# Kernel optimization log

Measured on AMD Instinct MI355X. Metric: run time of the kernel, lower is better.

The kernel has to match this reference:

```python
import jax, jax.numpy as jnp
import numpy as np

N_NODES = 100000
N_EDGES = 1600000
N_GRAPHS = 512
F_IN = 20
HID = 128
OUT = HID // 2


def _glorot(key, shape):
    fan_in, fan_out = shape[0], shape[1]
    lim = float(np.sqrt(6.0 / (fan_in + fan_out)))
    return jax.random.uniform(key, shape, jnp.float32, -lim, lim)


def setup_inputs() -> dict:
    key = jax.random.key(0)
    ks = jax.random.split(key, 12)
    x = jax.random.normal(ks[0], (N_NODES, F_IN), jnp.float32)
    edge_index = jax.random.randint(ks[1], (2, N_EDGES), 0, N_NODES, dtype=jnp.int64)
    batch = jnp.sort(jax.random.randint(ks[2], (N_NODES,), 0, N_GRAPHS, dtype=jnp.int64))
    return {
        "x": x,
        "edge_index": edge_index,
        "batch": batch,
        "W1": _glorot(ks[3], (F_IN, HID)), "b1": jnp.zeros((HID,), jnp.float32),
        "W2": _glorot(ks[4], (HID, HID)), "b2": jnp.zeros((HID,), jnp.float32),
        "W3": _glorot(ks[5], (HID, HID)), "b3": jnp.zeros((HID,), jnp.float32),
        "Wout": _glorot(ks[6], (HID, OUT)), "bout": jnp.zeros((OUT,), jnp.float32),
    }


def _gcn_conv(x, W, b, src, dst, num_nodes):
    # PyG GCNConv: x' = D^{-1/2} (A + I) D^{-1/2} X W + b (self-loops already in src/dst)
    xw = x @ W                                                  # [N, H]
    ones = jnp.ones(src.shape[0], dtype=xw.dtype)
    deg = jax.ops.segment_sum(ones, dst, num_segments=num_nodes)
    dinv = jnp.where(deg > 0, jax.lax.rsqrt(deg), 0.0)          # [N]
    norm = dinv[src] * dinv[dst]                                # [E+N]
    msg = xw[src] * norm[:, None]                               # gather + scale
    return jax.ops.segment_sum(msg, dst, num_segments=num_nodes) + b


def reference(x, edge_index, batch, W1, b1, W2, b2, W3, b3, Wout, bout):
    num_nodes = x.shape[0]
    loops = jnp.arange(num_nodes, dtype=edge_index.dtype)
    src = jnp.concatenate([edge_index[0], loops])
    dst = jnp.concatenate([edge_index[1], loops])

    h = jax.nn.relu(_gcn_conv(x, W1, b1, src, dst, num_nodes))
    h = jax.nn.relu(_gcn_conv(h, W2, b2, src, dst, num_nodes))
    h = jax.nn.relu(_gcn_conv(h, W3, b3, src, dst, num_nodes))

    # global_mean_pool over graph ids
    sums = jax.ops.segment_sum(h, batch, num_segments=N_GRAPHS)
    counts = jax.ops.segment_sum(jnp.ones(num_nodes, h.dtype), batch, num_segments=N_GRAPHS)
    pooled = sums / jnp.maximum(counts, 1.0)[:, None]           # [G, H]
    return pooled @ Wout + bout                                 # [G, H//2]
```

## Files before the change

kernel.cpp:

```cpp
#include <hip/hip_runtime.h>
#include <hip/hip_fp16.h>

#define N_NODES 100000
#define N_EDGES 1600000
#define N_GRAPHS 512
#define F_IN 20
#define HID 128
#define OUT_F 64

#define BUCKETS 256
#define SPAN 391
#define BCAP 7000
#define EPB 4096

typedef _Float16 half8_t __attribute__((ext_vector_type(8)));
typedef float f32x4_t __attribute__((ext_vector_type(4)));

__device__ inline float4 h4_to_f4(uint2 u) {
    __half2 h0 = *(__half2*)&u.x;
    __half2 h1 = *(__half2*)&u.y;
    float2 f0 = __half22float2(h0);
    float2 f1 = __half22float2(h1);
    return make_float4(f0.x, f0.y, f1.x, f1.y);
}

__global__ __launch_bounds__(512) void partition(const int* __restrict__ src,
                                                 const int* __restrict__ dst,
                                                 int* __restrict__ bpairs,
                                                 int* cur256) {
    __shared__ int lcnt[8][BUCKETS];
    __shared__ int woff[8][BUCKETS];
    int t = threadIdx.x;
    int wv = t >> 6;
    for (int i = t; i < 8 * BUCKETS; i += 512) ((int*)lcnt)[i] = 0;
    __syncthreads();
    int base = blockIdx.x * EPB;
    int myb[8], myp[8], myr[8];
#pragma unroll
    for (int i = 0; i < 8; ++i) {
        int e = base + i * 512 + t;
        int b = -1, p = 0, rk = 0;
        if (e < N_EDGES) {
            int s = src[e], d = dst[e];
            b = d / SPAN;
            p = (s << 9) | (d - b * SPAN);
            rk = atomicAdd(&lcnt[wv][b], 1);
        }
        myb[i] = b; myp[i] = p; myr[i] = rk;
    }
    __syncthreads();
    if (t < BUCKETS) {
        int c[8], tot = 0;
#pragma unroll
        for (int w = 0; w < 8; ++w) { c[w] = lcnt[w][t]; tot += c[w]; }
        int gb = atomicAdd(&cur256[t], tot);
#pragma unroll
        for (int w = 0; w < 8; ++w) { woff[w][t] = gb; gb += c[w]; }
    }
    __syncthreads();
#pragma unroll
    for (int i = 0; i < 8; ++i) {
        int b = myb[i];
        if (b >= 0) {
            int p = woff[wv][b] + myr[i];
            if (p < BCAP) bpairs[(size_t)b * BCAP + p] = myp[i];
        }
    }
}

__global__ __launch_bounds__(512) void csr_build(const int* __restrict__ bpairs,
                                                 const int* __restrict__ cur256,
                                                 int* __restrict__ row_st,
                                                 int* __restrict__ csr,
                                                 const float* __restrict__ x,
                                                 __half* __restrict__ Xs) {
    __shared__ int ocnt[SPAN];
    __shared__ int sc[512];
    __shared__ int cur[SPAN];
    __shared__ int sbase;
    int b = blockIdx.x, t = threadIdx.x;

    int myc = (t < BUCKETS) ? cur256[t] : 0;
    sc[t] = myc;
    __syncthreads();
    for (int o = 1; o < BUCKETS; o <<= 1) {
        int v = (t >= o) ? sc[t - o] : 0;
        __syncthreads();
        sc[t] += v;
        __syncthreads();
    }
    if (t == b) sbase = sc[t] - myc;
    if (b == BUCKETS - 1 && t == 0) row_st[N_NODES] = N_EDGES;

    int n0 = b * SPAN;
    int span = N_NODES - n0; if (span > SPAN) span = SPAN;
    if (t < SPAN) ocnt[t] = 0;
    __syncthreads();

    int n = cur256[b];
    const int* p = bpairs + (size_t)b * BCAP;
    for (int i = t; i < n; i += 512) atomicAdd(&ocnt[p[i] & 511], 1);
    __syncthreads();
    sc[t] = (t < span) ? ocnt[t] : 0;
    __syncthreads();
    for (int o = 1; o < 512; o <<= 1) {
        int v = (t >= o) ? sc[t - o] : 0;
        __syncthreads();
        sc[t] += v;
        __syncthreads();
    }
    int base = sbase;
    if (t < span) {
        int start = sc[t] - ocnt[t];
        row_st[n0 + t] = base + start;
        cur[t] = start;
    }
    __syncthreads();
    for (int i = t; i < n; i += 512) {
        int e = p[i];
        int lp = atomicAdd(&cur[e & 511], 1);
        csr[base + lp] = e >> 9;
    }
    for (int i = t; i < span * 32; i += 512) {
        int nl = i >> 5, f = i & 31;
        float v = (f < F_IN) ? x[(size_t)(n0 + nl) * F_IN + f] : 0.f;
        float di = rsqrtf((float)(ocnt[nl] + 1));
        Xs[(size_t)(n0 + nl) * 32 + f] = __float2half(di * v);
    }
}

__global__ __launch_bounds__(256) void layer1(const __half* __restrict__ Xs,
                                              const int* __restrict__ row_st,
                                              const int* __restrict__ csr,
                                              const float* __restrict__ W,
                                              const float* __restrict__ bias,
                                              __half* __restrict__ H) {
    __shared__ float Wlds[F_IN * HID];
    __shared__ float Alds[16 * F_IN];
    const int t = threadIdx.x;
    const int node0 = blockIdx.x * 16;

    for (int i = t; i < F_IN * HID; i += 256) Wlds[i] = W[i];

    const int h16 = t >> 4;
    const int l16 = t & 15;
    const __half2* X2 = (const __half2*)Xs;
    {
        int nn = node0 + h16;
        int r0 = row_st[nn], r1 = row_st[nn + 1];
        float2 f = __half22float2(X2[(size_t)nn * 16 + l16]);
        float2 acc = f;
        int r = r0;
        for (; r + 1 < r1; r += 2) {
            float2 f0 = __half22float2(X2[(size_t)csr[r] * 16 + l16]);
            float2 f1 = __half22float2(X2[(size_t)csr[r + 1] * 16 + l16]);
            acc.x += f0.x + f1.x;
            acc.y += f0.y + f1.y;
        }
        if (r < r1) {
            float2 f2 = __half22float2(X2[(size_t)csr[r] * 16 + l16]);
            acc.x += f2.x; acc.y += f2.y;
        }
        if (l16 < 10) {
            float di = rsqrtf((float)(r1 - r0 + 1));
            Alds[h16 * F_IN + l16 * 2]     = di * acc.x;
            Alds[h16 * F_IN + l16 * 2 + 1] = di * acc.y;
        }
    }
    __syncthreads();

    const int g  = t >> 5;
    const int h4 = (t & 31) * 4;
    float4 b4 = *(const float4*)&bias[h4];
    float4 acc0 = b4;
    float4 acc1 = b4;
#pragma unroll
    for (int kk = 0; kk < F_IN; ++kk) {
        float a0 = Alds[(g * 2) * F_IN + kk];
        float a1 = Alds[(g * 2 + 1) * F_IN + kk];
        float4 w = *(const float4*)&Wlds[kk * HID + h4];
        acc0.x = fmaf(a0, w.x, acc0.x);
        acc0.y = fmaf(a0, w.y, acc0.y);
        acc0.z = fmaf(a0, w.z, acc0.z);
        acc0.w = fmaf(a0, w.w, acc0.w);
        acc1.x = fmaf(a1, w.x, acc1.x);
        acc1.y = fmaf(a1, w.y, acc1.y);
        acc1.z = fmaf(a1, w.z, acc1.z);
        acc1.w = fmaf(a1, w.w, acc1.w);
    }
    {
        __half2 h0 = __floats2half2_rn(acc0.x, acc0.y);
        __half2 h1 = __floats2half2_rn(acc0.z, acc0.w);
        uint2 u; u.x = *(unsigned*)&h0; u.y = *(unsigned*)&h1;
        ((uint2*)H)[(node0 + g * 2) * 32 + (h4 >> 2)] = u;
    }
    {
        __half2 h0 = __floats2half2_rn(acc1.x, acc1.y);
        __half2 h1 = __floats2half2_rn(acc1.z, acc1.w);
        uint2 u; u.x = *(unsigned*)&h0; u.y = *(unsigned*)&h1;
        ((uint2*)H)[(node0 + g * 2 + 1) * 32 + (h4 >> 2)] = u;
    }
}

__global__ __launch_bounds__(256) void gemm_mfma(const __half* __restrict__ H,
                                                 const float* __restrict__ W,
                                                 const int* __restrict__ row_st,
                                                 __half* __restrict__ T) {
    __shared__ _Float16 Whi[64 * 128];
    __shared__ _Float16 Wlo[64 * 128];
    const int t = threadIdx.x;
    const int c0 = (blockIdx.x & 1) * 64;

    for (int i = t; i < 128 * 64; i += 256) {
        int k = i >> 6, c = i & 63;
        float w = W[k * HID + c0 + c];
        _Float16 hi = (_Float16)w;
        _Float16 lo = (_Float16)((w - (float)hi) * 2048.0f);
        int addr = c * 128 + (((k >> 3) ^ (c & 15)) << 3) + (k & 7);
        Whi[addr] = hi;
        Wlo[addr] = lo;
    }
    __syncthreads();

    const int wv = t >> 6;
    const int l  = t & 63;
    const int lr = l & 15;
    const int lq = l >> 4;

    for (int rep = 0; rep < 4; ++rep) {
        int strip = ((blockIdx.x >> 1) * 4 + wv) * 4 + rep;
        if (strip >= N_NODES / 16) continue;
        int n0 = strip * 16;

        f32x4_t acc[4], acl[4];
#pragma unroll
        for (int ct = 0; ct < 4; ++ct) { acc[ct] = (f32x4_t){0,0,0,0}; acl[ct] = (f32x4_t){0,0,0,0}; }

#pragma unroll
        for (int kc = 0; kc < 4; ++kc) {
            half8_t a = *(const half8_t*)(H + (size_t)(n0 + lr) * 128 + kc * 32 + lq * 8);
#pragma unroll
            for (int j = 0; j < 8; ++j) a[j] = a[j] > (_Float16)0 ? a[j] : (_Float16)0;
            int g = kc * 4 + lq;
#pragma unroll
            for (int ct = 0; ct < 4; ++ct) {
                int c = ct * 16 + lr;
                int addr = c * 128 + ((g ^ lr) << 3);
                half8_t bh = *(const half8_t*)&Whi[addr];
                half8_t bl = *(const half8_t*)&Wlo[addr];
                acc[ct] = __builtin_amdgcn_mfma_f32_16x16x32_f16(a, bh, acc[ct], 0, 0, 0);
                acl[ct] = __builtin_amdgcn_mfma_f32_16x16x32_f16(a, bl, acl[ct], 0, 0, 0);
            }
        }

        int r0 = n0 + lq * 4;
#pragma unroll
        for (int r = 0; r < 4; ++r) {
            int row = r0 + r;
            float d = rsqrtf((float)(row_st[row + 1] - row_st[row] + 1));
#pragma unroll
            for (int ct = 0; ct < 4; ++ct) {
                float v = (acc[ct][r] + acl[ct][r] * 4.8828125e-4f) * d;
                T[(size_t)row * 128 + c0 + ct * 16 + lr] = __float2half(v);
            }
        }
    }
}

__global__ __launch_bounds__(256) void gather_range(const __half* __restrict__ A,
                                                    const int* __restrict__ row_st,
                                                    const int* __restrict__ csr,
                                                    const float* __restrict__ bias,
                                                    __half* __restrict__ B) {
    int t = threadIdx.x;
    int n = blockIdx.x * 8 + (t >> 5);
    int l = t & 31;
    int r0 = row_st[n], r1 = row_st[n + 1];
    float di = rsqrtf((float)(r1 - r0 + 1));
    const uint2* Af = (const uint2*)A;
    float4 acc = h4_to_f4(Af[n * 32 + l]);
    int r = r0;
    for (; r + 7 < r1; r += 8) {
        int s0 = csr[r],     s1 = csr[r + 1], s2 = csr[r + 2], s3 = csr[r + 3];
        int s4 = csr[r + 4], s5 = csr[r + 5], s6 = csr[r + 6], s7 = csr[r + 7];
        float4 v0 = h4_to_f4(Af[s0 * 32 + l]);
        float4 v1 = h4_to_f4(Af[s1 * 32 + l]);
        float4 v2 = h4_to_f4(Af[s2 * 32 + l]);
        float4 v3 = h4_to_f4(Af[s3 * 32 + l]);
        float4 v4 = h4_to_f4(Af[s4 * 32 + l]);
        float4 v5 = h4_to_f4(Af[s5 * 32 + l]);
        float4 v6 = h4_to_f4(Af[s6 * 32 + l]);
        float4 v7 = h4_to_f4(Af[s7 * 32 + l]);
        acc.x += ((v0.x + v1.x) + (v2.x + v3.x)) + ((v4.x + v5.x) + (v6.x + v7.x));
        acc.y += ((v0.y + v1.y) + (v2.y + v3.y)) + ((v4.y + v5.y) + (v6.y + v7.y));
        acc.z += ((v0.z + v1.z) + (v2.z + v3.z)) + ((v4.z + v5.z) + (v6.z + v7.z));
        acc.w += ((v0.w + v1.w) + (v2.w + v3.w)) + ((v4.w + v5.w) + (v6.w + v7.w));
    }
    for (; r + 3 < r1; r += 4) {
        int s0 = csr[r], s1 = csr[r + 1], s2 = csr[r + 2], s3 = csr[r + 3];
        float4 v0 = h4_to_f4(Af[s0 * 32 + l]);
        float4 v1 = h4_to_f4(Af[s1 * 32 + l]);
        float4 v2 = h4_to_f4(Af[s2 * 32 + l]);
        float4 v3 = h4_to_f4(Af[s3 * 32 + l]);
        acc.x += (v0.x + v1.x) + (v2.x + v3.x);
        acc.y += (v0.y + v1.y) + (v2.y + v3.y);
        acc.z += (v0.z + v1.z) + (v2.z + v3.z);
        acc.w += (v0.w + v1.w) + (v2.w + v3.w);
    }
    for (; r < r1; ++r) {
        float4 v = h4_to_f4(Af[csr[r] * 32 + l]);
        acc.x += v.x; acc.y += v.y; acc.z += v.z; acc.w += v.w;
    }
    float4 b4 = ((const float4*)bias)[l];
    __half2 h0 = __floats2half2_rn(fmaf(di, acc.x, b4.x), fmaf(di, acc.y, b4.y));
    __half2 h1 = __floats2half2_rn(fmaf(di, acc.z, b4.z), fmaf(di, acc.w, b4.w));
    uint2 u; u.x = *(unsigned*)&h0; u.y = *(unsigned*)&h1;
    ((uint2*)B)[n * 32 + l] = u;
}

__global__ __launch_bounds__(256) void gather_pool(const __half* __restrict__ A,
                                                   const int* __restrict__ row_st,
                                                   const int* __restrict__ csr,
                                                   const float* __restrict__ bias,
                                                   const int* __restrict__ batch,
                                                   float* sums, float* counts) {
    int t = threadIdx.x;
    int l = t & 31;
    int n0 = (blockIdx.x * 8 + (t >> 5)) * 8;
    if (n0 >= N_NODES) return;
    const uint2* Af = (const uint2*)A;
    float4 b4 = ((const float4*)bias)[l];
    int cur = batch[n0];
    int runlen = 0;
    float4 pacc = make_float4(0.f, 0.f, 0.f, 0.f);
    for (int k = 0; k < 8; ++k) {
        int n = n0 + k;
        if (n >= N_NODES) break;
        int g = batch[n];
        if (g != cur) {
            float* sp = &sums[cur * HID + l * 4];
            atomicAdd(sp + 0, pacc.x); atomicAdd(sp + 1, pacc.y);
            atomicAdd(sp + 2, pacc.z); atomicAdd(sp + 3, pacc.w);
            if (l == 0) atomicAdd(&counts[cur], (float)runlen);
            pacc = make_float4(0.f, 0.f, 0.f, 0.f);
            runlen = 0;
            cur = g;
        }
        int r0 = row_st[n], r1 = row_st[n + 1];
        float4 acc = h4_to_f4(Af[n * 32 + l]);
        int r = r0;
        for (; r + 7 < r1; r += 8) {
            int s0 = csr[r],     s1 = csr[r + 1], s2 = csr[r + 2], s3 = csr[r + 3];
            int s4 = csr[r + 4], s5 = csr[r + 5], s6 = csr[r + 6], s7 = csr[r + 7];
            float4 v0 = h4_to_f4(Af[s0 * 32 + l]);
            float4 v1 = h4_to_f4(Af[s1 * 32 + l]);
            float4 v2 = h4_to_f4(Af[s2 * 32 + l]);
            float4 v3 = h4_to_f4(Af[s3 * 32 + l]);
            float4 v4 = h4_to_f4(Af[s4 * 32 + l]);
            float4 v5 = h4_to_f4(Af[s5 * 32 + l]);
            float4 v6 = h4_to_f4(Af[s6 * 32 + l]);
            float4 v7 = h4_to_f4(Af[s7 * 32 + l]);
            acc.x += ((v0.x + v1.x) + (v2.x + v3.x)) + ((v4.x + v5.x) + (v6.x + v7.x));
            acc.y += ((v0.y + v1.y) + (v2.y + v3.y)) + ((v4.y + v5.y) + (v6.y + v7.y));
            acc.z += ((v0.z + v1.z) + (v2.z + v3.z)) + ((v4.z + v5.z) + (v6.z + v7.z));
            acc.w += ((v0.w + v1.w) + (v2.w + v3.w)) + ((v4.w + v5.w) + (v6.w + v7.w));
        }
        for (; r + 3 < r1; r += 4) {
            int s0 = csr[r], s1 = csr[r + 1], s2 = csr[r + 2], s3 = csr[r + 3];
            float4 v0 = h4_to_f4(Af[s0 * 32 + l]);
            float4 v1 = h4_to_f4(Af[s1 * 32 + l]);
            float4 v2 = h4_to_f4(Af[s2 * 32 + l]);
            float4 v3 = h4_to_f4(Af[s3 * 32 + l]);
            acc.x += (v0.x + v1.x) + (v2.x + v3.x);
            acc.y += (v0.y + v1.y) + (v2.y + v3.y);
            acc.z += (v0.z + v1.z) + (v2.z + v3.z);
            acc.w += (v0.w + v1.w) + (v2.w + v3.w);
        }
        for (; r < r1; ++r) {
            float4 v = h4_to_f4(Af[csr[r] * 32 + l]);
            acc.x += v.x; acc.y += v.y; acc.z += v.z; acc.w += v.w;
        }
        float di = rsqrtf((float)(r1 - r0 + 1));
        pacc.x += fmaxf(fmaf(di, acc.x, b4.x), 0.f);
        pacc.y += fmaxf(fmaf(di, acc.y, b4.y), 0.f);
        pacc.z += fmaxf(fmaf(di, acc.z, b4.z), 0.f);
        pacc.w += fmaxf(fmaf(di, acc.w, b4.w), 0.f);
        ++runlen;
    }
    float* sp = &sums[cur * HID + l * 4];
    atomicAdd(sp + 0, pacc.x); atomicAdd(sp + 1, pacc.y);
    atomicAdd(sp + 2, pacc.z); atomicAdd(sp + 3, pacc.w);
    if (l == 0) atomicAdd(&counts[cur], (float)runlen);
}

__global__ void final_gemm(const float* __restrict__ sums, const float* __restrict__ counts,
                           const float* __restrict__ Wout, const float* __restrict__ bout,
                           float* __restrict__ out) {
    int g = blockIdx.x;
    int o = threadIdx.x;
    __shared__ float p[HID];
    for (int k = o; k < HID; k += 64) p[k] = sums[g * HID + k];
    __syncthreads();
    float inv = 1.0f / fmaxf(counts[g], 1.0f);
    float acc = 0.f;
#pragma unroll 8
    for (int k = 0; k < HID; ++k)
        acc = fmaf(p[k], Wout[k * OUT_F + o], acc);
    out[g * OUT_F + o] = fmaf(inv, acc, bout[o]);
}

extern "C" void kernel_launch(void* const* d_in, const int* in_sizes, int n_in,
                              void* d_out, int out_size, void* d_ws, size_t ws_size,
                              hipStream_t stream) {
    const float* x     = (const float*)d_in[0];
    const int*   ei    = (const int*)d_in[1];
    const int*   batch = (const int*)d_in[2];
    const float* W1    = (const float*)d_in[3];
    const float* b1    = (const float*)d_in[4];
    const float* W2    = (const float*)d_in[5];
    const float* b2    = (const float*)d_in[6];
    const float* W3    = (const float*)d_in[7];
    const float* b3    = (const float*)d_in[8];
    const float* Wout  = (const float*)d_in[9];
    const float* bout  = (const float*)d_in[10];
    float* out = (float*)d_out;

    const int* src = ei;
    const int* dst = ei + N_EDGES;

    float* A      = (float*)d_ws;
    float* Breg   = A + (size_t)N_NODES * HID;
    int*   row_st = (int*)(Breg + (size_t)N_NODES * HID);
    float* sums   = (float*)(row_st + N_NODES + 1);
    float* counts = sums + N_GRAPHS * HID;
    int*   cur256 = (int*)(counts + N_GRAPHS);
    int*   csr    = cur256 + BUCKETS;

    int*    bpairs = (int*)A;
    __half* Xs     = (__half*)((char*)A + 7168000);
    __half* T      = (__half*)A;
    __half* H      = (__half*)Breg;

    hipMemsetAsync(sums, 0, (size_t)(N_GRAPHS * HID + N_GRAPHS + BUCKETS) * 4, stream);
    partition<<<(N_EDGES + EPB - 1) / EPB, 512, 0, stream>>>(src, dst, bpairs, cur256);
    csr_build<<<BUCKETS, 512, 0, stream>>>(bpairs, cur256, row_st, csr, x, Xs);

    layer1<<<N_NODES / 16, 256, 0, stream>>>(Xs, row_st, csr, W1, b1, H);

    gemm_mfma<<<782, 256, 0, stream>>>(H, W2, row_st, T);
    gather_range<<<N_NODES / 8, 256, 0, stream>>>(T, row_st, csr, b2, H);
    gemm_mfma<<<782, 256, 0, stream>>>(H, W3, row_st, T);
    gather_pool<<<(N_NODES + 63) / 64, 256, 0, stream>>>(T, row_st, csr, b3, batch, sums, counts);

    final_gemm<<<N_GRAPHS, 64, 0, stream>>>(sums, counts, Wout, bout, out);
}
```

Baseline: 373.5 us.

## Double CSR buckets and give gather_pool one node per half-wave with shared-memory pooling

The edge partition now uses 512 buckets of 196 nodes each, which halves per-bucket capacity and doubles the number of csr_build blocks. Out-of-range span and count values are clamped. gather_pool is restructured so each group of 32 lanes handles one node instead of eight sequential nodes. Results are staged in shared memory and a single warp does the run-length pooling and atomics per block. The aim is more parallelism and latency hiding in the final gather and the CSR build, at the cost of an extra block sync and more blocks. The smaller bucket capacity also risks overflow if a bucket gets unusually many edges.

New measurement: 360.2 us. 3.6% less time.

```diff
diff --git a/kernel.cpp b/kernel.cpp
--- a/kernel.cpp
+++ b/kernel.cpp
@@ -8,9 +8,9 @@
 #define HID 128
 #define OUT_F 64
 
-#define BUCKETS 256
-#define SPAN 391
-#define BCAP 7000
+#define BUCKETS 512
+#define SPAN 196
+#define BCAP 3500
 #define EPB 4096
 
 typedef _Float16 half8_t __attribute__((ext_vector_type(8)));
@@ -27,7 +27,7 @@
 __global__ __launch_bounds__(512) void partition(const int* __restrict__ src,
                                                  const int* __restrict__ dst,
                                                  int* __restrict__ bpairs,
-                                                 int* cur256) {
+                                                 int* cur512) {
     __shared__ int lcnt[8][BUCKETS];
     __shared__ int woff[8][BUCKETS];
     int t = threadIdx.x;
@@ -49,11 +49,11 @@
         myb[i] = b; myp[i] = p; myr[i] = rk;
     }
     __syncthreads();
-    if (t < BUCKETS) {
+    {
         int c[8], tot = 0;
 #pragma unroll
         for (int w = 0; w < 8; ++w) { c[w] = lcnt[w][t]; tot += c[w]; }
-        int gb = atomicAdd(&cur256[t], tot);
+        int gb = atomicAdd(&cur512[t], tot);
 #pragma unroll
         for (int w = 0; w < 8; ++w) { woff[w][t] = gb; gb += c[w]; }
     }
@@ -69,7 +69,7 @@
 }
 
 __global__ __launch_bounds__(512) void csr_build(const int* __restrict__ bpairs,
-                                                 const int* __restrict__ cur256,
+                                                 const int* __restrict__ cur512,
                                                  int* __restrict__ row_st,
                                                  int* __restrict__ csr,
                                                  const float* __restrict__ x,
@@ -80,7 +80,7 @@
     __shared__ int sbase;
     int b = blockIdx.x, t = threadIdx.x;
 
-    int myc = (t < BUCKETS) ? cur256[t] : 0;
+    int myc = cur512[t];
     sc[t] = myc;
     __syncthreads();
     for (int o = 1; o < BUCKETS; o <<= 1) {
@@ -94,10 +94,12 @@
 
     int n0 = b * SPAN;
     int span = N_NODES - n0; if (span > SPAN) span = SPAN;
+    if (span < 0) span = 0;
     if (t < SPAN) ocnt[t] = 0;
     __syncthreads();
 
-    int n = cur256[b];
+    int n = cur512[b];
+    if (n > BCAP) n = BCAP;
     const int* p = bpairs + (size_t)b * BCAP;
     for (int i = t; i < n; i += 512) atomicAdd(&ocnt[p[i] & 511], 1);
     __syncthreads();
@@ -324,73 +326,82 @@
                                                    const float* __restrict__ bias,
                                                    const int* __restrict__ batch,
                                                    float* sums, float* counts) {
+    __shared__ float4 rbuf[8][32];
+    __shared__ int rgid[8];
     int t = threadIdx.x;
+    int g = t >> 5;
+    int n = blockIdx.x * 8 + g;
     int l = t & 31;
-    int n0 = (blockIdx.x * 8 + (t >> 5)) * 8;
-    if (n0 >= N_NODES) return;
+    int r0 = row_st[n], r1 = row_st[n + 1];
+    float di = rsqrtf((float)(r1 - r0 + 1));
     const uint2* Af = (const uint2*)A;
+    float4 acc = h4_to_f4(Af[n * 32 + l]);
+    int r = r0;
+    for (; r + 7 < r1; r += 8) {
+        int s0 = csr[r],     s1 = csr[r + 1], s2 = csr[r + 2], s3 = csr[r + 3];
+        int s4 = csr[r + 4], s5 = csr[r + 5], s6 = csr[r + 6], s7 = csr[r + 7];
+        float4 v0 = h4_to_f4(Af[s0 * 32 + l]);
+        float4 v1 = h4_to_f4(Af[s1 * 32 + l]);
+        float4 v2 = h4_to_f4(Af[s2 * 32 + l]);
+        float4 v3 = h4_to_f4(Af[s3 * 32 + l]);
+        float4 v4 = h4_to_f4(Af[s4 * 32 + l]);
+        float4 v5 = h4_to_f4(Af[s5 * 32 + l]);
+        float4 v6 = h4_to_f4(Af[s6 * 32 + l]);
+        float4 v7 = h4_to_f4(Af[s7 * 32 + l]);
+        acc.x += ((v0.x + v1.x) + (v2.x + v3.x)) + ((v4.x + v5.x) + (v6.x + v7.x));
+        acc.y += ((v0.y + v1.y) + (v2.y + v3.y)) + ((v4.y + v5.y) + (v6.y + v7.y));
+        acc.z += ((v0.z + v1.z) + (v2.z + v3.z)) + ((v4.z + v5.z) + (v6.z + v7.z));
+        acc.w += ((v0.w + v1.w) + (v2.w + v3.w)) + ((v4.w + v5.w) + (v6.w + v7.w));
+    }
+    for (; r + 3 < r1; r += 4) {
+        int s0 = csr[r], s1 = csr[r + 1], s2 = csr[r + 2], s3 = csr[r + 3];
+        float4 v0 = h4_to_f4(Af[s0 * 32 + l]);
+        float4 v1 = h4_to_f4(Af[s1 * 32 + l]);
+        float4 v2 = h4_to_f4(Af[s2 * 32 + l]);
+        float4 v3 = h4_to_f4(Af[s3 * 32 + l]);
+        acc.x += (v0.x + v1.x) + (v2.x + v3.x);
+        acc.y += (v0.y + v1.y) + (v2.y + v3.y);
+        acc.z += (v0.z + v1.z) + (v2.z + v3.z);
+        acc.w += (v0.w + v1.w) + (v2.w + v3.w);
+    }
+    for (; r < r1; ++r) {
+        float4 v = h4_to_f4(Af[csr[r] * 32 + l]);
+        acc.x += v.x; acc.y += v.y; acc.z += v.z; acc.w += v.w;
+    }
     float4 b4 = ((const float4*)bias)[l];
-    int cur = batch[n0];
-    int runlen = 0;
-    float4 pacc = make_float4(0.f, 0.f, 0.f, 0.f);
-    for (int k = 0; k < 8; ++k) {
-        int n = n0 + k;
-        if (n >= N_NODES) break;
-        int g = batch[n];
-        if (g != cur) {
-            float* sp = &sums[cur * HID + l * 4];
-            atomicAdd(sp + 0, pacc.x); atomicAdd(sp + 1, pacc.y);
-            atomicAdd(sp + 2, pacc.z); atomicAdd(sp + 3, pacc.w);
-            if (l == 0) atomicAdd(&counts[cur], (float)runlen);
-            pacc = make_float4(0.f, 0.f, 0.f, 0.f);
-            runlen = 0;
-            cur = g;
-        }
-        int r0 = row_st[n], r1 = row_st[n + 1];
-        float4 acc = h4_to_f4(Af[n * 32 + l]);
-        int r = r0;
-        for (; r + 7 < r1; r += 8) {
-            int s0 = csr[r],     s1 = csr[r + 1], s2 = csr[r + 2], s3 = csr[r + 3];
-            int s4 = csr[r + 4], s5 = csr[r + 5], s6 = csr[r + 6], s7 = csr[r + 7];
-            float4 v0 = h4_to_f4(Af[s0 * 32 + l]);
-            float4 v1 = h4_to_f4(Af[s1 * 32 + l]);
-            float4 v2 = h4_to_f4(Af[s2 * 32 + l]);
-            float4 v3 = h4_to_f4(Af[s3 * 32 + l]);
-            float4 v4 = h4_to_f4(Af[s4 * 32 + l]);
-            float4 v5 = h4_to_f4(Af[s5 * 32 + l]);
-            float4 v6 = h4_to_f4(Af[s6 * 32 + l]);
-            float4 v7 = h4_to_f4(Af[s7 * 32 + l]);
-            acc.x += ((v0.x + v1.x) + (v2.x + v3.x)) + ((v4.x + v5.x) + (v6.x + v7.x));
-            acc.y += ((v0.y + v1.y) + (v2.y + v3.y)) + ((v4.y + v5.y) + (v6.y + v7.y));
-            acc.z += ((v0.z + v1.z) + (v2.z + v3.z)) + ((v4.z + v5.z) + (v6.z + v7.z));
-            acc.w += ((v0.w + v1.w) + (v2.w + v3.w)) + ((v4.w + v5.w) + (v6.w + v7.w));
-        }
-        for (; r + 3 < r1; r += 4) {
-            int s0 = csr[r], s1 = csr[r + 1], s2 = csr[r + 2], s3 = csr[r + 3];
-            float4 v0 = h4_to_f4(Af[s0 * 32 + l]);
-            float4 v1 = h4_to_f4(Af[s1 * 32 + l]);
-            float4 v2 = h4_to_f4(Af[s2 * 32 + l]);
-            float4 v3 = h4_to_f4(Af[s3 * 32 + l]);
-            acc.x += (v0.x + v1.x) + (v2.x + v3.x);
-            acc.y += (v0.y + v1.y) + (v2.y + v3.y);
-            acc.z += (v0.z + v1.z) + (v2.z + v3.z);
-            acc.w += (v0.w + v1.w) + (v2.w + v3.w);
-        }
-        for (; r < r1; ++r) {
-            float4 v = h4_to_f4(Af[csr[r] * 32 + l]);
-            acc.x += v.x; acc.y += v.y; acc.z += v.z; acc.w += v.w;
-        }
-        float di = rsqrtf((float)(r1 - r0 + 1));
-        pacc.x += fmaxf(fmaf(di, acc.x, b4.x), 0.f);
-        pacc.y += fmaxf(fmaf(di, acc.y, b4.y), 0.f);
-        pacc.z += fmaxf(fmaf(di, acc.z, b4.z), 0.f);
-        pacc.w += fmaxf(fmaf(di, acc.w, b4.w), 0.f);
-        ++runlen;
-    }
-    float* sp = &sums[cur * HID + l * 4];
-    atomicAdd(sp + 0, pacc.x); atomicAdd(sp + 1, pacc.y);
-    atomicAdd(sp + 2, pacc.z); atomicAdd(sp + 3, pacc.w);
-    if (l == 0) atomicAdd(&counts[cur], (float)runlen);
+    float4 o;
+    o.x = fmaxf(fmaf(di, acc.x, b4.x), 0.f);
+    o.y = fmaxf(fmaf(di, acc.y, b4.y), 0.f);
+    o.z = fmaxf(fmaf(di, acc.z, b4.z), 0.f);
+    o.w = fmaxf(fmaf(di, acc.w, b4.w), 0.f);
+    rbuf[g][l] = o;
+    if (l == 0) rgid[g] = batch[n];
+    __syncthreads();
+
+    if (t < 32) {
+        int cur = rgid[0];
+        float4 p = rbuf[0][t];
+        int runlen = 1;
+        for (int j = 1; j < 8; ++j) {
+            int g2 = rgid[j];
+            if (g2 != cur) {
+                float* sp = &sums[cur * HID + t * 4];
+                atomicAdd(sp + 0, p.x); atomicAdd(sp + 1, p.y);
+                atomicAdd(sp + 2, p.z); atomicAdd(sp + 3, p.w);
+                if (t == 0) atomicAdd(&counts[cur], (float)runlen);
+                p = make_float4(0.f, 0.f, 0.f, 0.f);
+                runlen = 0;
+                cur = g2;
+            }
+            float4 v = rbuf[j][t];
+            p.x += v.x; p.y += v.y; p.z += v.z; p.w += v.w;
+            ++runlen;
+        }
+        float* sp = &sums[cur * HID + t * 4];
+        atomicAdd(sp + 0, p.x); atomicAdd(sp + 1, p.y);
+        atomicAdd(sp + 2, p.z); atomicAdd(sp + 3, p.w);
+        if (t == 0) atomicAdd(&counts[cur], (float)runlen);
+    }
 }
 
 __global__ void final_gemm(const float* __restrict__ sums, const float* __restrict__ counts,
@@ -433,8 +444,8 @@
     int*   row_st = (int*)(Breg + (size_t)N_NODES * HID);
     float* sums   = (float*)(row_st + N_NODES + 1);
     float* counts = sums + N_GRAPHS * HID;
-    int*   cur256 = (int*)(counts + N_GRAPHS);
-    int*   csr    = cur256 + BUCKETS;
+    int*   cur512 = (int*)(counts + N_GRAPHS);
+    int*   csr    = cur512 + BUCKETS;
 
     int*    bpairs = (int*)A;
     __half* Xs     = (__half*)((char*)A + 7168000);
@@ -442,15 +453,15 @@
     __half* H      = (__half*)Breg;
 
     hipMemsetAsync(sums, 0, (size_t)(N_GRAPHS * HID + N_GRAPHS + BUCKETS) * 4, stream);
-    partition<<<(N_EDGES + EPB - 1) / EPB, 512, 0, stream>>>(src, dst, bpairs, cur256);
-    csr_build<<<BUCKETS, 512, 0, stream>>>(bpairs, cur256, row_st, csr, x, Xs);
+    partition<<<(N_EDGES + EPB - 1) / EPB, 512, 0, stream>>>(src, dst, bpairs, cur512);
+    csr_build<<<BUCKETS, 512, 0, stream>>>(bpairs, cur512, row_st, csr, x, Xs);
 
     layer1<<<N_NODES / 16, 256, 0, stream>>>(Xs, row_st, csr, W1, b1, H);
 
     gemm_mfma<<<782, 256, 0, stream>>>(H, W2, row_st, T);
     gather_range<<<N_NODES / 8, 256, 0, stream>>>(T, row_st, csr, b2, H);
     gemm_mfma<<<782, 256, 0, stream>>>(H, W3, row_st, T);
-    gather_pool<<<(N_NODES + 63) / 64, 256, 0, stream>>>(T, row_st, csr, b3, batch, sums, counts);
+    gather_pool<<<N_NODES / 8, 256, 0, stream>>>(T, row_st, csr, b3, batch, sums, counts);
 
     final_gemm<<<N_GRAPHS, 64, 0, stream>>>(sums, counts, Wout, bout, out);
 }
```
